# Kernel optimization log

Measured on AMD Instinct MI355X. Metric: run time of the kernel, lower is better.

## Reference

```python
import math
import jax, jax.numpy as jnp
import numpy as np

S = 2048      # seq_length
D = 1024      # embedding_dim
H = 16        # num_qkv_heads
HD = D // H   # head_size = 64
L = 4         # num_hidden_layers
V = 32000     # vocab_size
EPS = 1e-5    # nn.LayerNorm default eps


def setup_inputs() -> dict:
    key = jax.random.key(0)
    ks = jax.random.split(key, 16)
    def n(k, shape, scale=0.02):
        return (jax.random.normal(k, shape, jnp.float32) * scale)
    return {
        "input_ids": jax.random.randint(ks[0], (S,), 0, V),
        "embed":     n(ks[1], (V, D)),
        "pos_enc":   n(ks[2], (S, D)),
        # per-layer stacked params; nn.Linear stores W as [out, in]
        "wq": n(ks[3], (L, D, D)), "bq": jnp.zeros((L, D), jnp.float32),
        "wk": n(ks[4], (L, D, D)), "bk": jnp.zeros((L, D), jnp.float32),
        "wv": n(ks[5], (L, D, D)), "bv": jnp.zeros((L, D), jnp.float32),
        "wo": n(ks[6], (L, D, D)), "bo": jnp.zeros((L, D), jnp.float32),
        "ln1_g": jnp.ones((L, D), jnp.float32), "ln1_b": jnp.zeros((L, D), jnp.float32),
        "w1": n(ks[7], (L, 4 * D, D)), "b1": jnp.zeros((L, 4 * D), jnp.float32),
        "w2": n(ks[8], (L, D, 4 * D)), "b2": jnp.zeros((L, D), jnp.float32),
        "ln2_g": jnp.ones((L, D), jnp.float32), "ln2_b": jnp.zeros((L, D), jnp.float32),
        "lm_head": n(ks[9], (V, D)),
    }


def _layer_norm(x, g, b):
    mu = jnp.mean(x, axis=-1, keepdims=True)
    var = jnp.mean(jnp.square(x - mu), axis=-1, keepdims=True)
    return (x - mu) * jax.lax.rsqrt(var + EPS) * g + b


def _forward(input_ids, embed, pos_enc, wq, bq, wk, bk, wv, bv, wo, bo,
             ln1_g, ln1_b, w1, b1, w2, b2, ln2_g, ln2_b, lm_head):
    s = input_ids.shape[0]
    h = embed[input_ids] + pos_enc[:s]                      # [S, D]
    causal = jnp.tril(jnp.ones((s, s), dtype=bool))         # [S, S]
    inv_sqrt_dk = 1.0 / math.sqrt(HD)

    def layer(h, p):
        (lwq, lbq, lwk, lbk, lwv, lbv, lwo, lbo,
         g1, bn1, lw1, lb1, lw2, lb2, g2, bn2) = p
        q = (h @ lwq.T + lbq).reshape(s, H, HD).transpose(1, 0, 2)  # [H, S, HD]
        k = (h @ lwk.T + lbk).reshape(s, H, HD).transpose(1, 0, 2)
        v = (h @ lwv.T + lbv).reshape(s, H, HD).transpose(1, 0, 2)
        scores = jnp.einsum('hqd,hkd->hqk', q, k) * inv_sqrt_dk     # [H, S, S]
        scores = jnp.where(causal, scores, -jnp.inf)
        attn = jax.nn.softmax(scores, axis=-1)
        o = jnp.einsum('hqk,hkd->hqd', attn, v)                     # [H, S, HD]
        o = o.transpose(1, 0, 2).reshape(s, D) @ lwo.T + lbo        # [S, D]
        h = _layer_norm(h + o, g1, bn1)
        m = jax.nn.relu(h @ lw1.T + lb1) @ lw2.T + lb2              # [S, D]
        h = _layer_norm(h + m, g2, bn2)
        return h, None

    h, _ = jax.lax.scan(layer, h, (wq, bq, wk, bk, wv, bv, wo, bo,
                                   ln1_g, ln1_b, w1, b1, w2, b2, ln2_g, ln2_b))
    return h @ lm_head.T                                    # [S, V] logits


def reference(input_ids, embed, pos_enc, wq, bq, wk, bk, wv, bv, wo, bo,
              ln1_g, ln1_b, w1, b1, w2, b2, ln2_g, ln2_b, lm_head):
    return _forward(input_ids, embed, pos_enc, wq, bq, wk, bk, wv, bv, wo, bo,
                    ln1_g, ln1_b, w1, b1, w2, b2, ln2_g, ln2_b, lm_head)
```

## Files before the change

kernel.cpp:

```cpp
#include <hip/hip_runtime.h>
#include <hip/hip_bf16.h>

#define S 2048
#define D 1024
#define NH 16
#define HD 64
#define NL 4
#define VOCAB 32000
#define DFF 4096
#define EPS_LN 1e-5f

typedef unsigned short ushortT;
typedef __attribute__((ext_vector_type(8))) short short8;
typedef __attribute__((ext_vector_type(4))) unsigned short ushort4v;
typedef __attribute__((ext_vector_type(4))) float f32x4;

__device__ __forceinline__ ushortT f2bf(float f) {
    unsigned u = __float_as_uint(f);
    u += 0x7FFFu + ((u >> 16) & 1u);
    return (ushortT)(u >> 16);
}

__device__ __forceinline__ void gload_lds16(const ushortT* g, ushortT* l) {
    auto gp = (const __attribute__((address_space(1))) unsigned int*)(uintptr_t)g;
    auto lp = (__attribute__((address_space(3))) unsigned int*)(uintptr_t)l;
    __builtin_amdgcn_global_load_lds(gp, lp, 16, 0, 0);
}

__device__ __forceinline__ void cvt8(const float* s, ushortT* d) {
    float4 a = *(const float4*)s;
    float4 b = *(const float4*)(s + 4);
    short8 r;
    r[0] = (short)f2bf(a.x); r[1] = (short)f2bf(a.y);
    r[2] = (short)f2bf(a.z); r[3] = (short)f2bf(a.w);
    r[4] = (short)f2bf(b.x); r[5] = (short)f2bf(b.y);
    r[6] = (short)f2bf(b.z); r[7] = (short)f2bf(b.w);
    *(short8*)d = r;
}

__global__ __launch_bounds__(256) void embed_kernel(
    const int* __restrict__ ids, const float* __restrict__ embed,
    const float* __restrict__ pos, float* __restrict__ hf, ushortT* __restrict__ hb)
{
    int i = blockIdx.x * 256 + threadIdx.x;
    int srow = i >> 10;
    int d = i & (D - 1);
    float v = embed[(size_t)ids[srow] * D + d] + pos[i];
    hf[i] = v;
    hb[i] = f2bf(v);
}

__global__ __launch_bounds__(256) void convert_layer(
    const float* __restrict__ wq, const float* __restrict__ wk, const float* __restrict__ wv,
    const float* __restrict__ wo, const float* __restrict__ w1, const float* __restrict__ w2,
    const float* __restrict__ bq, const float* __restrict__ bk, const float* __restrict__ bv,
    int l, ushortT* __restrict__ wl, float* __restrict__ bqkv)
{
    constexpr int R = (D * D) / 8;
    const int u = blockIdx.x * 256 + threadIdx.x;
    if (u < 12 * R) {
        const float* src;
        if (u < 3 * R) {
            int sub = u >> 17, off = u & (R - 1);
            const float* w = (sub == 0) ? wq : (sub == 1) ? wk : wv;
            src = w + (size_t)l * D * D + (size_t)off * 8;
        } else if (u < 4 * R) {
            src = wo + (size_t)l * D * D + (size_t)(u - 3 * R) * 8;
        } else if (u < 8 * R) {
            src = w1 + (size_t)l * 4 * D * D + (size_t)(u - 4 * R) * 8;
        } else {
            src = w2 + (size_t)l * 4 * D * D + (size_t)(u - 8 * R) * 8;
        }
        cvt8(src, wl + (size_t)u * 8);
    } else if (u < 12 * R + 384) {
        int i = u - 12 * R;
        int sub = i >> 7, off = (i & 127) * 8;
        const float* src = ((sub == 0) ? bq : (sub == 1) ? bk : bv) + (size_t)l * D + off;
        *(float4*)(bqkv + sub * D + off)     = *(const float4*)src;
        *(float4*)(bqkv + sub * D + off + 4) = *(const float4*)(src + 4);
    }
}

__global__ __launch_bounds__(256) void convert_flat(
    const float* __restrict__ src, ushortT* __restrict__ dst)
{
    const size_t u = (size_t)blockIdx.x * 256 + threadIdx.x;
    cvt8(src + u * 8, dst + u * 8);
}

template<int BN, int OUTMODE, int RELU, int HASBIAS>
__global__ __launch_bounds__(256) void gemm_bf(
    const ushortT* __restrict__ A, const ushortT* __restrict__ B,
    const float* __restrict__ bias, void* __restrict__ Cn, void* __restrict__ Ct,
    int N, int K)
{
    constexpr int WN = BN / 2;
    constexpr int NCT = WN / 16;
    __shared__ alignas(16) ushortT As[128 * 32];
    __shared__ alignas(16) ushortT Bs[BN * 32];

    const int tid = threadIdx.x;
    const int id = blockIdx.x;
    const int brow = (id & 15) * 128;
    const int bcol = (id >> 4) * BN;
    const int lane = tid & 63, wid = tid >> 6;
    const int l15 = lane & 15, l4 = lane >> 4;
    const int wr = wid >> 1, wc = wid & 1;
    const int str = tid >> 2;
    const int stc = (tid & 3) * 8;

    f32x4 acc[4][NCT] = {};

    const ushortT* Ab = A + (size_t)(brow + str) * K + stc;
    const ushortT* Bb = B + (size_t)(bcol + str) * K + stc;
    ushortT* AsD = &As[tid * 8];
    ushortT* BsD = &Bs[tid * 8];

    const int nkb = K >> 5;
    for (int kb = 0; kb < nkb; ++kb) {
        const int ko = kb * 32;
        gload_lds16(Ab + ko, AsD);
        gload_lds16(Ab + ko + (size_t)64 * K, AsD + 2048);
        gload_lds16(Bb + ko, BsD);
        if (BN == 128) gload_lds16(Bb + ko + (size_t)64 * K, BsD + 2048);
        __syncthreads();

        short8 af[4], bfr[NCT];
        #pragma unroll
        for (int rt = 0; rt < 4; ++rt)
            af[rt] = *(const short8*)&As[(wr * 64 + rt * 16 + l15) * 32 + l4 * 8];
        #pragma unroll
        for (int ct = 0; ct < NCT; ++ct)
            bfr[ct] = *(const short8*)&Bs[(wc * WN + ct * 16 + l15) * 32 + l4 * 8];
        #pragma unroll
        for (int rt = 0; rt < 4; ++rt)
            #pragma unroll
            for (int ct = 0; ct < NCT; ++ct)
                acc[rt][ct] = __builtin_amdgcn_mfma_f32_16x16x32_bf16(af[rt], bfr[ct], acc[rt][ct], 0, 0, 0);
        __syncthreads();
    }

    #pragma unroll
    for (int rt = 0; rt < 4; ++rt) {
        const int crow0 = brow + wr * 64 + rt * 16 + l4 * 4;
        #pragma unroll
        for (int ct = 0; ct < NCT; ++ct) {
            const int ccol = bcol + wc * WN + ct * 16 + l15;
            const float bv = HASBIAS ? bias[ccol] : 0.0f;
            if (OUTMODE == 0) {
                float* C = (float*)Cn;
                #pragma unroll
                for (int j = 0; j < 4; ++j) {
                    float v = acc[rt][ct][j] + bv;
                    if (RELU) v = fmaxf(v, 0.0f);
                    C[(size_t)(crow0 + j) * N + ccol] = v;
                }
            } else if (OUTMODE == 1) {
                ushortT* C = (ushortT*)Cn;
                #pragma unroll
                for (int j = 0; j < 4; ++j) {
                    float v = acc[rt][ct][j] + bv;
                    if (RELU) v = fmaxf(v, 0.0f);
                    C[(size_t)(crow0 + j) * N + ccol] = f2bf(v);
                }
            }
        }
    }
}

__global__ __launch_bounds__(512) void gemm_lmhead(
    const ushortT* __restrict__ A, const ushortT* __restrict__ B,
    float* __restrict__ C, int N)
{
    constexpr int K = 1024;
    constexpr int NT = K >> 6;
    __shared__ alignas(128) ushortT lds[65536];

    const int tid = threadIdx.x;
    const int NB = N >> 8;
    const int bid = blockIdx.x;
    const int wgid = (bid & 7) * (NB >> 3) * 8 / 8 * 8 + 0;
    (void)wgid;
    const int cpx = gridDim.x >> 3;
    const int wg = (bid & 7) * cpx + (bid >> 3);
    const int brow = (wg & 7) << 8;
    const int bcol = (wg >> 3) << 8;

    const int lane = tid & 63;
    const int wid = tid >> 6;
    const int l15 = lane & 15, l4 = lane >> 4;
    const int wm = wid >> 2, wn = wid & 3;

    const int srow = tid >> 3;
    const int scol = ((tid & 7) ^ (srow & 7)) * 8;
    const ushortT* Asrc = A + (size_t)(brow + srow) * K + scol;
    const ushortT* Bsrc = B + (size_t)(bcol + srow) * K + scol;

    auto stA = [&](int t, int h) {
        if (t < NT) {
            const int bb = t & 1;
            #pragma unroll
            for (int g = 0; g < 2; ++g)
                gload_lds16(Asrc + (size_t)(h * 128 + g * 64) * K + (size_t)t * 64,
                            &lds[bb * 32768 + h * 8192 + g * 4096 + tid * 8]);
        }
    };
    auto stB = [&](int t, int h) {
        if (t < NT) {
            const int bb = t & 1;
            #pragma unroll
            for (int g = 0; g < 2; ++g)
                gload_lds16(Bsrc + (size_t)(h * 128 + g * 64) * K + (size_t)t * 64,
                            &lds[bb * 32768 + 16384 + h * 8192 + g * 4096 + tid * 8]);
        }
    };

    f32x4 acc[2][2][4][2] = {};

    stA(0, 0); stB(0, 0); stA(0, 1); stB(0, 1); stB(1, 0); stA(1, 0);
    asm volatile("s_waitcnt vmcnt(4)" ::: "memory");
    __builtin_amdgcn_s_barrier();

#define RD_A(DST, RC)                                                          \
    _Pragma("unroll") for (int r16 = 0; r16 < 4; ++r16)                        \
    _Pragma("unroll") for (int kk = 0; kk < 2; ++kk)                           \
        DST[r16][kk] = *(const short8*)&lds[b * 32768 +                        \
            (((RC) * 128 + wm * 64 + r16 * 16 + l15) << 6) +                   \
            ((((kk << 2) + l4) ^ (l15 & 7)) << 3)];
#define RD_B(DST, CC)                                                          \
    _Pragma("unroll") for (int c16 = 0; c16 < 2; ++c16)                        \
    _Pragma("unroll") for (int kk = 0; kk < 2; ++kk)                           \
        DST[c16][kk] = *(const short8*)&lds[b * 32768 + 16384 +                \
            (((CC) * 128 + wn * 32 + c16 * 16 + l15) << 6) +                   \
            ((((kk << 2) + l4) ^ (l15 & 7)) << 3)];
#define MFMA_Q(AF, BF, RC, CC)                                                 \
    __builtin_amdgcn_s_setprio(1);                                             \
    _Pragma("unroll") for (int kk = 0; kk < 2; ++kk)                           \
    _Pragma("unroll") for (int r16 = 0; r16 < 4; ++r16)                        \
    _Pragma("unroll") for (int c16 = 0; c16 < 2; ++c16)                        \
        acc[RC][CC][r16][c16] = __builtin_amdgcn_mfma_f32_16x16x32_bf16(       \
            BF[c16][kk], AF[r16][kk], acc[RC][CC][r16][c16], 0, 0, 0);         \
    __builtin_amdgcn_s_setprio(0);
#define WAIT_LGKM                                                              \
    asm volatile("s_waitcnt lgkmcnt(0)" ::: "memory");                         \
    __builtin_amdgcn_sched_barrier(0);

    for (int t = 0; t < NT; ++t) {
        const int b = t & 1;
        short8 a_[4][2], b0[2][2], b1[2][2];

        RD_A(a_, 0); RD_B(b0, 0);
        stA(t + 1, 1);
        __builtin_amdgcn_s_barrier();
        WAIT_LGKM;
        MFMA_Q(a_, b0, 0, 0);
        __builtin_amdgcn_s_barrier();

        RD_B(b1, 1);
        stB(t + 1, 1);
        __builtin_amdgcn_s_barrier();
        WAIT_LGKM;
        MFMA_Q(a_, b1, 0, 1);
        __builtin_amdgcn_s_barrier();

        RD_A(a_, 1);
        stB(t + 2, 0);
        __builtin_amdgcn_s_barrier();
        WAIT_LGKM;
        MFMA_Q(a_, b1, 1, 1);
        __builtin_amdgcn_s_barrier();

        stA(t + 2, 0);
        __builtin_amdgcn_s_barrier();
        MFMA_Q(a_, b0, 1, 0);
        if (t < NT - 2) { asm volatile("s_waitcnt vmcnt(4)" ::: "memory"); }
        else            { asm volatile("s_waitcnt vmcnt(0)" ::: "memory"); }
        __builtin_amdgcn_s_barrier();
    }
#undef RD_A
#undef RD_B
#undef MFMA_Q
#undef WAIT_LGKM

    #pragma unroll
    for (int rc = 0; rc < 2; ++rc)
    #pragma unroll
    for (int cc = 0; cc < 2; ++cc)
    #pragma unroll
    for (int r16 = 0; r16 < 4; ++r16)
    #pragma unroll
    for (int c16 = 0; c16 < 2; ++c16) {
        const int row = brow + rc * 128 + wm * 64 + r16 * 16 + l15;
        const int col = bcol + cc * 128 + wn * 32 + c16 * 16 + l4 * 4;
        __builtin_nontemporal_store(acc[rc][cc][r16][c16],
                                    (f32x4*)&C[(size_t)row * N + col]);
    }
}

template<int OUTMODE, int RELU, int HASBIAS, int SWAP>
__global__ __launch_bounds__(512) void gemm256v(
    const ushortT* __restrict__ A, const ushortT* __restrict__ B,
    const float* __restrict__ bias, void* __restrict__ Cn, void* __restrict__ Ct,
    int N, int NBn, int Kloop, int stride)
{
    __shared__ alignas(128) ushortT lds[73728];

    const int tid = threadIdx.x;
    const int bid = blockIdx.x;
    const int cpx = gridDim.x >> 3;
    const int wgid = (bid & 7) * cpx + (bid >> 3);
    const int brow = (wgid & 7) << 8;
    const int rest = wgid >> 3;
    const int split = rest / NBn;
    const int bcol = (rest - split * NBn) << 7;
    const int kofs = split * Kloop;

    const int lane = tid & 63, wid = tid >> 6;
    const int l15 = lane & 15, l4 = lane >> 4;
    const int wm = wid >> 1, wn = wid & 1;
    const int NT = Kloop >> 6;

    const int srow = tid >> 3;
    const int scol = ((tid & 7) ^ (srow & 7)) * 8;
    const ushortT* Asrc = A + (size_t)(brow + srow) * stride + kofs + scol;
    const ushortT* Bsrc = B + (size_t)(bcol + srow) * stride + kofs + scol;

    auto stA = [&](int t, int h) {
        if (t < NT) {
            const int sb = t % 3;
            #pragma unroll
            for (int g = 0; g < 2; ++g)
                gload_lds16(Asrc + (size_t)(h * 128 + g * 64) * stride + (size_t)t * 64,
                            &lds[sb * 24576 + h * 8192 + g * 4096 + tid * 8]);
        }
    };
    auto stB = [&](int t) {
        if (t < NT) {
            const int sb = t % 3;
            #pragma unroll
            for (int g = 0; g < 2; ++g)
                gload_lds16(Bsrc + (size_t)(g * 64) * stride + (size_t)t * 64,
                            &lds[sb * 24576 + 16384 + g * 4096 + tid * 8]);
        }
    };

    f32x4 acc[4][4] = {};

    stA(0, 0); stA(0, 1); stB(0);
    stA(1, 0); stA(1, 1); stB(1);
    asm volatile("s_waitcnt vmcnt(6)" ::: "memory");
    __builtin_amdgcn_s_barrier();

    for (int t = 0; t < NT; ++t) {
        const unsigned abase = (unsigned)(t % 3) * 24576;
        short8 af[4][2], bf2[2][2];

        #pragma unroll
        for (int r16 = 0; r16 < 4; ++r16)
            #pragma unroll
            for (int kk = 0; kk < 2; ++kk)
                af[r16][kk] = *(const short8*)&lds[abase +
                    ((wm * 64 + r16 * 16 + l15) << 6) +
                    ((((kk << 2) + l4) ^ (l15 & 7)) << 3)];
        #pragma unroll
        for (int c16 = 0; c16 < 2; ++c16)
            #pragma unroll
            for (int kk = 0; kk < 2; ++kk)
                bf2[c16][kk] = *(const short8*)&lds[abase + 16384 +
                    ((wn * 64 + c16 * 16 + l15) << 6) +
                    ((((kk << 2) + l4) ^ (l15 & 7)) << 3)];
        stA(t + 2, 0); stA(t + 2, 1);
        __builtin_amdgcn_s_barrier();
        asm volatile("s_waitcnt lgkmcnt(0)" ::: "memory");
        __builtin_amdgcn_sched_barrier(0);
        __builtin_amdgcn_s_setprio(1);
        #pragma unroll
        for (int kk = 0; kk < 2; ++kk)
            #pragma unroll
            for (int r16 = 0; r16 < 4; ++r16)
                #pragma unroll
                for (int c16 = 0; c16 < 2; ++c16)
                    acc[r16][c16] = SWAP
                        ? __builtin_amdgcn_mfma_f32_16x16x32_bf16(bf2[c16][kk], af[r16][kk], acc[r16][c16], 0, 0, 0)
                        : __builtin_amdgcn_mfma_f32_16x16x32_bf16(af[r16][kk], bf2[c16][kk], acc[r16][c16], 0, 0, 0);
        __builtin_amdgcn_s_setprio(0);
        __builtin_amdgcn_s_barrier();

        #pragma unroll
        for (int c16 = 0; c16 < 2; ++c16)
            #pragma unroll
            for (int kk = 0; kk < 2; ++kk)
                bf2[c16][kk] = *(const short8*)&lds[abase + 16384 +
                    ((wn * 64 + (c16 + 2) * 16 + l15) << 6) +
                    ((((kk << 2) + l4) ^ (l15 & 7)) << 3)];
        stB(t + 2);
        __builtin_amdgcn_s_barrier();
        asm volatile("s_waitcnt lgkmcnt(0)" ::: "memory");
        __builtin_amdgcn_sched_barrier(0);
        __builtin_amdgcn_s_setprio(1);
        #pragma unroll
        for (int kk = 0; kk < 2; ++kk)
            #pragma unroll
            for (int r16 = 0; r16 < 4; ++r16)
                #pragma unroll
                for (int c16 = 0; c16 < 2; ++c16)
                    acc[r16][c16 + 2] = SWAP
                        ? __builtin_amdgcn_mfma_f32_16x16x32_bf16(bf2[c16][kk], af[r16][kk], acc[r16][c16 + 2], 0, 0, 0)
                        : __builtin_amdgcn_mfma_f32_16x16x32_bf16(af[r16][kk], bf2[c16][kk], acc[r16][c16 + 2], 0, 0, 0);
        __builtin_amdgcn_s_setprio(0);
        if (t + 2 < NT) { asm volatile("s_waitcnt vmcnt(6)" ::: "memory"); }
        else            { asm volatile("s_waitcnt vmcnt(0)" ::: "memory"); }
        __builtin_amdgcn_s_barrier();
    }

    #pragma unroll
    for (int r16 = 0; r16 < 4; ++r16)
    #pragma unroll
    for (int c16 = 0; c16 < 4; ++c16) {
        if (SWAP) {
            const int row = brow + wm * 64 + r16 * 16 + l15;
            const int col = bcol + wn * 64 + c16 * 16 + l4 * 4;
            f32x4 v = acc[r16][c16];
            if (HASBIAS) {
                float4 b4 = *(const float4*)&bias[col];
                v[0] += b4.x; v[1] += b4.y; v[2] += b4.z; v[3] += b4.w;
            }
            if (RELU) {
                #pragma unroll
                for (int j = 0; j < 4; ++j) v[j] = fmaxf(v[j], 0.0f);
            }
            if (OUTMODE == 1) {
                ushort4v o;
                #pragma unroll
                for (int j = 0; j < 4; ++j) o[j] = f2bf(v[j]);
                *(ushort4v*)&((ushortT*)Cn)[(size_t)row * N + col] = o;
            } else if (OUTMODE == 3) {
                float* C = (float*)Cn + (size_t)split * 2048 * N;
                *(f32x4*)&C[(size_t)row * N + col] = v;
            } else {
                __builtin_nontemporal_store(v, (f32x4*)&((float*)Cn)[(size_t)row * N + col]);
            }
        } else {
            const int crow0 = brow + wm * 64 + r16 * 16 + l4 * 4;
            const int ccol  = bcol + wn * 64 + c16 * 16 + l15;
            const float bv = HASBIAS ? bias[ccol] : 0.0f;
            if (OUTMODE == 2) {
                if (ccol < 2048) {
                    ushortT* C = (ushortT*)Cn;
                    #pragma unroll
                    for (int j = 0; j < 4; ++j)
                        C[(size_t)(crow0 + j) * 2048 + ccol] = f2bf(acc[r16][c16][j] + bv);
                } else {
                    ushortT* C = (ushortT*)Ct;
                    ushort4v wv_;
                    #pragma unroll
                    for (int j = 0; j < 4; ++j) wv_[j] = f2bf(acc[r16][c16][j] + bv);
                    *(ushort4v*)&C[(size_t)(ccol - 2048) * S + crow0] = wv_;
                }
            } else if (OUTMODE == 1) {
                ushortT* C = (ushortT*)Cn;
                #pragma unroll
                for (int j = 0; j < 4; ++j) {
                    float v = acc[r16][c16][j] + bv;
                    if (RELU) v = fmaxf(v, 0.0f);
                    C[(size_t)(crow0 + j) * N + ccol] = f2bf(v);
                }
            } else {
                float* C = (float*)Cn;
                #pragma unroll
                for (int j = 0; j < 4; ++j) {
                    float v = acc[r16][c16][j] + bv;
                    if (RELU) v = fmaxf(v, 0.0f);
                    C[(size_t)(crow0 + j) * N + ccol] = v;
                }
            }
        }
    }
}

__global__ __launch_bounds__(256) void attn_kernel(
    const ushortT* __restrict__ qk, const ushortT* __restrict__ vt,
    ushortT* __restrict__ att)
{
    const int h = blockIdx.y;
    const int q0 = blockIdx.x * 64;
    const int tid = threadIdx.x;
    const int w = tid >> 6, lane = tid & 63;
    const int l15 = lane & 15, l4 = lane >> 4;
    const int qrow0 = q0 + w * 16;

    __shared__ short p_lds[4][16][48];

    short8 aq[2];
    {
        const ushortT* qp = qk + (size_t)(qrow0 + l15) * 2048 + h * HD + l4 * 8;
        aq[0] = *(const short8*)qp;
        aq[1] = *(const short8*)(qp + 32);
    }

    f32x4 o[4] = {};
    float mrow[4], lrow[4];
    #pragma unroll
    for (int j = 0; j < 4; ++j) { mrow[j] = -1e30f; lrow[j] = 0.0f; }

    const int nkb = blockIdx.x * 2 + 2;
    for (int kb32 = 0; kb32 < nkb; ++kb32) {
        const int kb = kb32 * 32;
        f32x4 s[2] = {};
        #pragma unroll
        for (int kh = 0; kh < 2; ++kh) {
            const ushortT* kp = qk + (size_t)(kb + kh * 16 + l15) * 2048 + 1024 + h * HD + l4 * 8;
            short8 b0 = *(const short8*)kp;
            short8 b1 = *(const short8*)(kp + 32);
            s[kh] = __builtin_amdgcn_mfma_f32_16x16x32_bf16(aq[0], b0, s[kh], 0, 0, 0);
            s[kh] = __builtin_amdgcn_mfma_f32_16x16x32_bf16(aq[1], b1, s[kh], 0, 0, 0);
        }
        float fac[4];
        #pragma unroll
        for (int j = 0; j < 4; ++j) {
            const int qg = qrow0 + l4 * 4 + j;
            float v0 = s[0][j] * 0.125f;
            float v1 = s[1][j] * 0.125f;
            if (kb + l15 > qg)      v0 = -1e30f;
            if (kb + 16 + l15 > qg) v1 = -1e30f;
            float bm = fmaxf(v0, v1);
            #pragma unroll
            for (int d_ = 1; d_ < 16; d_ <<= 1) bm = fmaxf(bm, __shfl_xor(bm, d_, 64));
            const float mnew = fmaxf(mrow[j], bm);
            const float f = __expf(mrow[j] - mnew);
            const float p0 = __expf(v0 - mnew);
            const float p1 = __expf(v1 - mnew);
            s[0][j] = p0; s[1][j] = p1;
            float rs = p0 + p1;
            #pragma unroll
            for (int d_ = 1; d_ < 16; d_ <<= 1) rs += __shfl_xor(rs, d_, 64);
            lrow[j] = lrow[j] * f + rs;
            mrow[j] = mnew;
            fac[j] = f;
        }
        #pragma unroll
        for (int c = 0; c < 4; ++c)
            #pragma unroll
            for (int j = 0; j < 4; ++j) o[c][j] *= fac[j];

        #pragma unroll
        for (int kh = 0; kh < 2; ++kh)
            #pragma unroll
            for (int j = 0; j < 4; ++j)
                p_lds[w][l4 * 4 + j][kh * 16 + l15] = (short)f2bf(s[kh][j]);
        short8 pa = *(const short8*)&p_lds[w][l15][l4 * 8];

        #pragma unroll
        for (int c = 0; c < 4; ++c) {
            short8 bv = *(const short8*)(vt + (size_t)(h * HD + c * 16 + l15) * S + kb + l4 * 8);
            o[c] = __builtin_amdgcn_mfma_f32_16x16x32_bf16(pa, bv, o[c], 0, 0, 0);
        }
    }

    #pragma unroll
    for (int c = 0; c < 4; ++c)
        #pragma unroll
        for (int j = 0; j < 4; ++j)
            att[(size_t)(qrow0 + l4 * 4 + j) * D + h * HD + c * 16 + l15] = f2bf(o[c][j] / lrow[j]);
}

template<int NP>
__global__ __launch_bounds__(256) void ln_kernel(
    const float* __restrict__ a,
    const float* __restrict__ p0, const float* __restrict__ p1,
    const float* __restrict__ p2, const float* __restrict__ p3,
    const float* __restrict__ pbias,
    const float* __restrict__ g, const float* __restrict__ bb,
    float* __restrict__ yf, ushortT* __restrict__ yb)
{
    const int row = blockIdx.x;
    const int tid = threadIdx.x;
    const size_t base = (size_t)row * D;
    float x[4]; float s = 0.f, s2 = 0.f;
    #pragma unroll
    for (int i = 0; i < 4; ++i) {
        const int c = tid + i * 256;
        float v = a[base + c] + p0[base + c] + pbias[c];
        if (NP > 1) v += p1[base + c] + p2[base + c] + p3[base + c];
        x[i] = v;
        s += v; s2 += v * v;
    }
    #pragma unroll
    for (int d_ = 1; d_ < 64; d_ <<= 1) {
        s  += __shfl_xor(s,  d_, 64);
        s2 += __shfl_xor(s2, d_, 64);
    }
    __shared__ float rs[4], rs2[4];
    const int wid = tid >> 6, lane = tid & 63;
    if (lane == 0) { rs[wid] = s; rs2[wid] = s2; }
    __syncthreads();
    s = rs[0] + rs[1] + rs[2] + rs[3];
    s2 = rs2[0] + rs2[1] + rs2[2] + rs2[3];
    const float mu = s * (1.0f / D);
    const float var = s2 * (1.0f / D) - mu * mu;
    const float inv = rsqrtf(var + EPS_LN);
    #pragma unroll
    for (int i = 0; i < 4; ++i) {
        const int c = tid + i * 256;
        float v = (x[i] - mu) * inv * g[c] + bb[c];
        yf[base + c] = v;
        yb[base + c] = f2bf(v);
    }
}

extern "C" void kernel_launch(void* const* d_in, const int* in_sizes, int n_in,
                              void* d_out, int out_size, void* d_ws, size_t ws_size,
                              hipStream_t stream) {
    const int*   ids   = (const int*)  d_in[0];
    const float* emb   = (const float*)d_in[1];
    const float* pos   = (const float*)d_in[2];
    const float* wq    = (const float*)d_in[3];
    const float* bq    = (const float*)d_in[4];
    const float* wk    = (const float*)d_in[5];
    const float* bk    = (const float*)d_in[6];
    const float* wv    = (const float*)d_in[7];
    const float* bv    = (const float*)d_in[8];
    const float* wo    = (const float*)d_in[9];
    const float* bo    = (const float*)d_in[10];
    const float* ln1g  = (const float*)d_in[11];
    const float* ln1b  = (const float*)d_in[12];
    const float* w1    = (const float*)d_in[13];
    const float* b1    = (const float*)d_in[14];
    const float* w2    = (const float*)d_in[15];
    const float* b2    = (const float*)d_in[16];
    const float* ln2g  = (const float*)d_in[17];
    const float* ln2b  = (const float*)d_in[18];
    const float* lmh   = (const float*)d_in[19];
    float* out = (float*)d_out;

    const size_t MB = 1024 * 1024;
    char* w = (char*)d_ws;
    float*   h_f32   = (float*)(w);
    float*   h2_f32  = (float*)(w +  8 * MB);
    float*   om2_f32 = (float*)(w + 16 * MB);
    ushortT* h_bf    = (ushortT*)(w + 24 * MB);
    ushortT* h2_bf   = (ushortT*)(w + 28 * MB);
    ushortT* qk_bf   = (ushortT*)(w + 32 * MB);
    ushortT* vt_bf   = (ushortT*)(w + 40 * MB);
    ushortT* att_bf  = (ushortT*)(w + 44 * MB);
    ushortT* m1_bf   = (ushortT*)(w + 48 * MB);
    ushortT* wl      = (ushortT*)(w + 64 * MB);
    float*   bqkv    = (float*)(w + 88 * MB);
    ushortT* lmh_bf  = (ushortT*)(w + 89 * MB);
    float*   parts   = (float*)(w + 155 * MB);

    const bool use_splitk = ws_size >= (size_t)187 * MB;

    ushortT* wqkv_bf = wl;
    ushortT* wo_bf   = wl + (size_t)3 * D * D;
    ushortT* w1_bf   = wl + (size_t)4 * D * D;
    ushortT* w2_bf   = wl + (size_t)8 * D * D;
    const size_t SD = (size_t)S * D;

    embed_kernel<<<(S * D) / 256, 256, 0, stream>>>(ids, emb, pos, h_f32, h_bf);

    for (int l = 0; l < NL; ++l) {
        convert_layer<<<6146, 256, 0, stream>>>(wq, wk, wv, wo, w1, w2, bq, bk, bv, l, wl, bqkv);

        gemm256v<2, 0, 1, 0><<<8 * 24, 512, 0, stream>>>(h_bf, wqkv_bf, bqkv, qk_bf, vt_bf,
                                                         3072, 24, D, D);

        attn_kernel<<<dim3(S / 64, NH), 256, 0, stream>>>(qk_bf, vt_bf, att_bf);

        gemm_bf<64, 0, 0, 0><<<16 * 16, 256, 0, stream>>>(att_bf, wo_bf, nullptr, om2_f32, nullptr, D, D);
        ln_kernel<1><<<S, 256, 0, stream>>>(h_f32, om2_f32, om2_f32, om2_f32, om2_f32,
                                            bo + (size_t)l * D,
                                            ln1g + (size_t)l * D, ln1b + (size_t)l * D, h2_f32, h2_bf);

        gemm256v<1, 1, 1, 1><<<8 * 32, 512, 0, stream>>>(h2_bf, w1_bf, b1 + (size_t)l * DFF, m1_bf, nullptr,
                                                         DFF, 32, D, D);

        if (use_splitk) {
            gemm256v<3, 0, 0, 1><<<8 * 8 * 4, 512, 0, stream>>>(m1_bf, w2_bf, nullptr, parts, nullptr,
                                                                D, 8, D, DFF);
            ln_kernel<4><<<S, 256, 0, stream>>>(h2_f32, parts, parts + SD, parts + 2 * SD, parts + 3 * SD,
                                                b2 + (size_t)l * D,
                                                ln2g + (size_t)l * D, ln2b + (size_t)l * D, h_f32, h_bf);
        } else {
            gemm_bf<64, 0, 0, 0><<<16 * 16, 256, 0, stream>>>(m1_bf, w2_bf, nullptr, om2_f32, nullptr, D, DFF);
            ln_kernel<1><<<S, 256, 0, stream>>>(h2_f32, om2_f32, om2_f32, om2_f32, om2_f32,
                                                b2 + (size_t)l * D,
                                                ln2g + (size_t)l * D, ln2b + (size_t)l * D, h_f32, h_bf);
        }
    }

    convert_flat<<<(VOCAB * D) / (256 * 8), 256, 0, stream>>>(lmh, lmh_bf);
    gemm_lmhead<<<8 * 125, 512, 0, stream>>>(h_bf, lmh_bf, out, VOCAB);
}
```

Baseline: 1.142 ms.

## Rewrite LM-head GEMM with 256x128 tiles, K=32 steps and triple buffering

Replaces the 256x256 LM-head GEMM tile, which used K=64 steps, double buffering and 128KB of LDS, with a 256x128 tile that uses K=32 steps, a three-stage LDS ring of about 72KB, and launch bounds that request higher occupancy. The grid doubles to 2000 workgroups. The aim is more resident workgroups and better latency hiding on a GEMM that writes a large output. In exchange, arithmetic intensity per tile drops, each tile loads A more often, and there are more barriers per K step.

```diff
diff --git a/kernel.cpp b/kernel.cpp
--- a/kernel.cpp
+++ b/kernel.cpp
@@ -168,132 +168,110 @@
     }
 }
 
-__global__ __launch_bounds__(512) void gemm_lmhead(
+__global__ __launch_bounds__(512, 4) void gemm_lm32(
     const ushortT* __restrict__ A, const ushortT* __restrict__ B,
     float* __restrict__ C, int N)
 {
     constexpr int K = 1024;
-    constexpr int NT = K >> 6;
-    __shared__ alignas(128) ushortT lds[65536];
+    constexpr int NT = 32;
+    __shared__ alignas(128) ushortT lds[36864];
 
     const int tid = threadIdx.x;
-    const int NB = N >> 8;
     const int bid = blockIdx.x;
-    const int wgid = (bid & 7) * (NB >> 3) * 8 / 8 * 8 + 0;
-    (void)wgid;
     const int cpx = gridDim.x >> 3;
     const int wg = (bid & 7) * cpx + (bid >> 3);
     const int brow = (wg & 7) << 8;
-    const int bcol = (wg >> 3) << 8;
-
-    const int lane = tid & 63;
-    const int wid = tid >> 6;
+    const int bcol = (wg >> 3) << 7;
+
+    const int lane = tid & 63, wid = tid >> 6;
     const int l15 = lane & 15, l4 = lane >> 4;
-    const int wm = wid >> 2, wn = wid & 3;
-
-    const int srow = tid >> 3;
-    const int scol = ((tid & 7) ^ (srow & 7)) * 8;
+    const int wm = wid >> 1, wn = wid & 1;
+    const int sw = (l15 & 3) ^ ((l15 >> 2) & 3);
+    const int chunk = (l4 ^ sw) << 3;
+
+    const int srow = tid >> 2;
+    const int scol = ((tid & 3) ^ ((srow & 3) ^ ((srow >> 2) & 3))) << 3;
     const ushortT* Asrc = A + (size_t)(brow + srow) * K + scol;
     const ushortT* Bsrc = B + (size_t)(bcol + srow) * K + scol;
 
     auto stA = [&](int t, int h) {
         if (t < NT) {
-            const int bb = t & 1;
-            #pragma unroll
-            for (int g = 0; g < 2; ++g)
-                gload_lds16(Asrc + (size_t)(h * 128 + g * 64) * K + (size_t)t * 64,
-                            &lds[bb * 32768 + h * 8192 + g * 4096 + tid * 8]);
+            const int sb = t % 3;
+            gload_lds16(Asrc + (size_t)(h * 128) * K + t * 32,
+                        &lds[sb * 12288 + h * 4096 + tid * 8]);
         }
     };
-    auto stB = [&](int t, int h) {
+    auto stB = [&](int t) {
         if (t < NT) {
-            const int bb = t & 1;
-            #pragma unroll
-            for (int g = 0; g < 2; ++g)
-                gload_lds16(Bsrc + (size_t)(h * 128 + g * 64) * K + (size_t)t * 64,
-                            &lds[bb * 32768 + 16384 + h * 8192 + g * 4096 + tid * 8]);
+            const int sb = t % 3;
+            gload_lds16(Bsrc + t * 32, &lds[sb * 12288 + 8192 + tid * 8]);
         }
     };
 
-    f32x4 acc[2][2][4][2] = {};
-
-    stA(0, 0); stB(0, 0); stA(0, 1); stB(0, 1); stB(1, 0); stA(1, 0);
-    asm volatile("s_waitcnt vmcnt(4)" ::: "memory");
+    f32x4 acc[4][4] = {};
+
+    stA(0, 0); stA(0, 1); stB(0);
+    stA(1, 0); stA(1, 1); stB(1);
+    asm volatile("s_waitcnt vmcnt(3)" ::: "memory");
     __builtin_amdgcn_s_barrier();
 
-#define RD_A(DST, RC)                                                          \
-    _Pragma("unroll") for (int r16 = 0; r16 < 4; ++r16)                        \
-    _Pragma("unroll") for (int kk = 0; kk < 2; ++kk)                           \
-        DST[r16][kk] = *(const short8*)&lds[b * 32768 +                        \
-            (((RC) * 128 + wm * 64 + r16 * 16 + l15) << 6) +                   \
-            ((((kk << 2) + l4) ^ (l15 & 7)) << 3)];
-#define RD_B(DST, CC)                                                          \
-    _Pragma("unroll") for (int c16 = 0; c16 < 2; ++c16)                        \
-    _Pragma("unroll") for (int kk = 0; kk < 2; ++kk)                           \
-        DST[c16][kk] = *(const short8*)&lds[b * 32768 + 16384 +                \
-            (((CC) * 128 + wn * 32 + c16 * 16 + l15) << 6) +                   \
-            ((((kk << 2) + l4) ^ (l15 & 7)) << 3)];
-#define MFMA_Q(AF, BF, RC, CC)                                                 \
-    __builtin_amdgcn_s_setprio(1);                                             \
-    _Pragma("unroll") for (int kk = 0; kk < 2; ++kk)                           \
-    _Pragma("unroll") for (int r16 = 0; r16 < 4; ++r16)                        \
-    _Pragma("unroll") for (int c16 = 0; c16 < 2; ++c16)                        \
-        acc[RC][CC][r16][c16] = __builtin_amdgcn_mfma_f32_16x16x32_bf16(       \
-            BF[c16][kk], AF[r16][kk], acc[RC][CC][r16][c16], 0, 0, 0);         \
-    __builtin_amdgcn_s_setprio(0);
-#define WAIT_LGKM                                                              \
-    asm volatile("s_waitcnt lgkmcnt(0)" ::: "memory");                         \
-    __builtin_amdgcn_sched_barrier(0);
-
     for (int t = 0; t < NT; ++t) {
-        const int b = t & 1;
-        short8 a_[4][2], b0[2][2], b1[2][2];
-
-        RD_A(a_, 0); RD_B(b0, 0);
-        stA(t + 1, 1);
-        __builtin_amdgcn_s_barrier();
-        WAIT_LGKM;
-        MFMA_Q(a_, b0, 0, 0);
-        __builtin_amdgcn_s_barrier();
-
-        RD_B(b1, 1);
-        stB(t + 1, 1);
-        __builtin_amdgcn_s_barrier();
-        WAIT_LGKM;
-        MFMA_Q(a_, b1, 0, 1);
-        __builtin_amdgcn_s_barrier();
-
-        RD_A(a_, 1);
-        stB(t + 2, 0);
-        __builtin_amdgcn_s_barrier();
-        WAIT_LGKM;
-        MFMA_Q(a_, b1, 1, 1);
-        __builtin_amdgcn_s_barrier();
-
-        stA(t + 2, 0);
-        __builtin_amdgcn_s_barrier();
-        MFMA_Q(a_, b0, 1, 0);
-        if (t < NT - 2) { asm volatile("s_waitcnt vmcnt(4)" ::: "memory"); }
+        const unsigned base = (unsigned)(t % 3) * 12288;
+        short8 af[4], bf2[2];
+
+        #pragma unroll
+        for (int r16 = 0; r16 < 4; ++r16) {
+            const int rr = (wm & 1) * 64 + r16 * 16 + l15;
+            af[r16] = *(const short8*)&lds[base + (wm >> 1) * 4096 + rr * 32 + chunk];
+        }
+        #pragma unroll
+        for (int c16 = 0; c16 < 2; ++c16) {
+            const int rr = wn * 64 + c16 * 16 + l15;
+            bf2[c16] = *(const short8*)&lds[base + 8192 + rr * 32 + chunk];
+        }
+        stA(t + 2, 0); stA(t + 2, 1);
+        __builtin_amdgcn_s_barrier();
+        asm volatile("s_waitcnt lgkmcnt(0)" ::: "memory");
+        __builtin_amdgcn_sched_barrier(0);
+        __builtin_amdgcn_s_setprio(1);
+        #pragma unroll
+        for (int r16 = 0; r16 < 4; ++r16)
+            #pragma unroll
+            for (int c16 = 0; c16 < 2; ++c16)
+                acc[r16][c16] = __builtin_amdgcn_mfma_f32_16x16x32_bf16(
+                    bf2[c16], af[r16], acc[r16][c16], 0, 0, 0);
+        __builtin_amdgcn_s_setprio(0);
+        __builtin_amdgcn_s_barrier();
+
+        #pragma unroll
+        for (int c16 = 0; c16 < 2; ++c16) {
+            const int rr = wn * 64 + (c16 + 2) * 16 + l15;
+            bf2[c16] = *(const short8*)&lds[base + 8192 + rr * 32 + chunk];
+        }
+        stB(t + 2);
+        __builtin_amdgcn_s_barrier();
+        asm volatile("s_waitcnt lgkmcnt(0)" ::: "memory");
+        __builtin_amdgcn_sched_barrier(0);
+        __builtin_amdgcn_s_setprio(1);
+        #pragma unroll
+        for (int r16 = 0; r16 < 4; ++r16)
+            #pragma unroll
+            for (int c16 = 0; c16 < 2; ++c16)
+                acc[r16][c16 + 2] = __builtin_amdgcn_mfma_f32_16x16x32_bf16(
+                    bf2[c16], af[r16], acc[r16][c16 + 2], 0, 0, 0);
+        __builtin_amdgcn_s_setprio(0);
+        if (t + 2 < NT) { asm volatile("s_waitcnt vmcnt(3)" ::: "memory"); }
         else            { asm volatile("s_waitcnt vmcnt(0)" ::: "memory"); }
         __builtin_amdgcn_s_barrier();
     }
-#undef RD_A
-#undef RD_B
-#undef MFMA_Q
-#undef WAIT_LGKM
-
-    #pragma unroll
-    for (int rc = 0; rc < 2; ++rc)
-    #pragma unroll
-    for (int cc = 0; cc < 2; ++cc)
+
     #pragma unroll
     for (int r16 = 0; r16 < 4; ++r16)
     #pragma unroll
-    for (int c16 = 0; c16 < 2; ++c16) {
-        const int row = brow + rc * 128 + wm * 64 + r16 * 16 + l15;
-        const int col = bcol + cc * 128 + wn * 32 + c16 * 16 + l4 * 4;
-        __builtin_nontemporal_store(acc[rc][cc][r16][c16],
-                                    (f32x4*)&C[(size_t)row * N + col]);
+    for (int c16 = 0; c16 < 4; ++c16) {
+        const int row = brow + wm * 64 + r16 * 16 + l15;
+        const int col = bcol + wn * 64 + c16 * 16 + l4 * 4;
+        __builtin_nontemporal_store(acc[r16][c16], (f32x4*)&C[(size_t)row * N + col]);
     }
 }
 
@@ -690,5 +668,5 @@
     }
 
     convert_flat<<<(VOCAB * D) / (256 * 8), 256, 0, stream>>>(lmh, lmh_bf);
-    gemm_lmhead<<<8 * 125, 512, 0, stream>>>(h_bf, lmh_bf, out, VOCAB);
-}
+    gemm_lm32<<<2000, 512, 0, stream>>>(h_bf, lmh_bf, out, VOCAB);
+}
```

Result: slower. 1.167 ms (+2.2%).
